# Performance work log

Measured on AMD Instinct MI355X. Metric: run time of the kernel, lower is better.

Reference implementation:

```python
import jax, jax.numpy as jnp
import numpy as np
import math

D = 1024      # input/embed dim
H = 16        # heads
HD = D // H   # head dim
FF = 4096     # feedforward dim
B, S = 2, 2048
LN_EPS = 1e-5
NEG = -9e15


def setup_inputs() -> dict:
    key = jax.random.key(0)
    ks = jax.random.split(key, 16)
    inp = {
        "x": jax.random.normal(ks[0], (B, S, D), jnp.float32),
        "mask": jax.random.randint(ks[1], (1, 1, S, S), 0, 2, jnp.int32),
        "pos_bias": jax.random.normal(ks[2], (1, H, S, S), jnp.float32),
        "sinusoidal_pos": jax.random.normal(ks[3], (1, 1, S, HD), jnp.float32),
        # params (xavier-ish scale)
        "Wqkv": jax.random.normal(ks[4], (D, 3 * D), jnp.float32) * math.sqrt(2.0 / (D + 3 * D)),
        "bqkv": jnp.zeros((3 * D,), jnp.float32),
        "Wo": jax.random.normal(ks[5], (D, D), jnp.float32) * math.sqrt(1.0 / D),
        "bo": jnp.zeros((D,), jnp.float32),
        "W1": jax.random.normal(ks[6], (D, FF), jnp.float32) * math.sqrt(2.0 / (D + FF)),
        "b1": jnp.zeros((FF,), jnp.float32),
        "W2": jax.random.normal(ks[7], (FF, D), jnp.float32) * math.sqrt(2.0 / (D + FF)),
        "b2": jnp.zeros((D,), jnp.float32),
        "g1": jnp.ones((D,), jnp.float32),
        "be1": jnp.zeros((D,), jnp.float32),
        "g2": jnp.ones((D,), jnp.float32),
        "be2": jnp.zeros((D,), jnp.float32),
    }
    return inp


def _layernorm(x, g, b):
    mu = jnp.mean(x, axis=-1, keepdims=True)
    var = jnp.mean(jnp.square(x - mu), axis=-1, keepdims=True)
    return (x - mu) * jax.lax.rsqrt(var + LN_EPS) * g + b


def _rotate_half(x):
    # x: [..., HD] -> reshape [..., 2, HD//2], swap with negation, concat
    r = x.reshape(*x.shape[:-1], 2, -1)
    x1, x2 = r[..., 0, :], r[..., 1, :]
    return jnp.concatenate([-x2, x1], axis=-1)


def _rope(x, sp):
    # sp: [1,1,S,HD]; x: [B,H,S,HD]
    return x * jnp.cos(sp) + _rotate_half(x) * jnp.sin(sp)


def reference(x, mask, pos_bias, sinusoidal_pos, Wqkv, bqkv, Wo, bo,
              W1, b1, W2, b2, g1, be1, g2, be2):
    # pre-norm (note: residual uses the normalized x, matching the source)
    x = _layernorm(x, g1, be1)
    b, s, d = x.shape
    qkv = (x @ Wqkv + bqkv).reshape(b, s, H, 3 * HD).transpose(0, 2, 1, 3)
    q, k, v = jnp.split(qkv, 3, axis=-1)  # each [B,H,S,HD]
    sp = sinusoidal_pos[:, :, -s:]
    q = _rope(q, sp)
    k = _rope(k, sp)
    logits = jnp.einsum("bhqd,bhkd->bhqk", q, k)
    logits = (logits + pos_bias) / math.sqrt(HD)
    logits = jnp.where(mask == 0, NEG, logits)
    attn = jax.nn.softmax(logits, axis=-1)
    vals = jnp.einsum("bhqk,bhkd->bhqd", attn, v)
    vals = vals.transpose(0, 2, 1, 3).reshape(b, s, d)
    attn_out = vals @ Wo + bo
    x = x + attn_out
    x = _layernorm(x, g2, be2)
    h = jax.nn.gelu(x @ W1 + b1, approximate=False)  # torch GELU is exact
    x = x + (h @ W2 + b2)
    return x
```

## Files before the change

kernel.cpp:

```cpp
#include <hip/hip_runtime.h>
#include <math.h>

#define DD   1024
#define HH   16
#define HDD  64
#define FFF  4096
#define NB   2
#define NS   2048
#define NR   (NB * NS)
#define TDQ  (3 * DD)
#define NKT  (NS / 64)

typedef __attribute__((ext_vector_type(8))) _Float16 hfrag;
typedef __attribute__((ext_vector_type(4))) _Float16 h4v;
typedef __attribute__((ext_vector_type(16))) float f32x16;
typedef __attribute__((ext_vector_type(8))) unsigned short us8;
typedef __attribute__((ext_vector_type(4))) unsigned int u32x4;

__device__ __forceinline__ float4 ld4(const float* p) {
    return *reinterpret_cast<const float4*>(p);
}
__device__ __forceinline__ float gelu_f(float x) {
    return 0.5f * x * (1.0f + erff(x * 0.70710678118654752440f));
}
#define MFMA32H(a, b, c) __builtin_amdgcn_mfma_f32_32x32x16_f16((a), (b), (c), 0, 0, 0)

__global__ __launch_bounds__(256) void ln_kernel(const float* __restrict__ in,
        const float* __restrict__ gw, const float* __restrict__ bw,
        float* __restrict__ outf, _Float16* __restrict__ oh) {
    int row = blockIdx.x;
    float4 v = reinterpret_cast<const float4*>(in + (size_t)row * DD)[threadIdx.x];
    float s1 = v.x + v.y + v.z + v.w;
    float s2 = v.x * v.x + v.y * v.y + v.z * v.z + v.w * v.w;
#pragma unroll
    for (int off = 1; off < 64; off <<= 1) {
        s1 += __shfl_xor(s1, off);
        s2 += __shfl_xor(s2, off);
    }
    __shared__ float r1[4], r2[4];
    int wid = threadIdx.x >> 6;
    if ((threadIdx.x & 63) == 0) { r1[wid] = s1; r2[wid] = s2; }
    __syncthreads();
    s1 = r1[0] + r1[1] + r1[2] + r1[3];
    s2 = r2[0] + r2[1] + r2[2] + r2[3];
    float mu   = s1 * (1.0f / DD);
    float var  = s2 * (1.0f / DD) - mu * mu;
    float rstd = rsqrtf(var + 1e-5f);
    float4 g = reinterpret_cast<const float4*>(gw)[threadIdx.x];
    float4 b = reinterpret_cast<const float4*>(bw)[threadIdx.x];
    float o[4];
    o[0] = (v.x - mu) * rstd * g.x + b.x;
    o[1] = (v.y - mu) * rstd * g.y + b.y;
    o[2] = (v.z - mu) * rstd * g.z + b.z;
    o[3] = (v.w - mu) * rstd * g.w + b.w;
    float4 of; of.x = o[0]; of.y = o[1]; of.z = o[2]; of.w = o[3];
    reinterpret_cast<float4*>(outf + (size_t)row * DD)[threadIdx.x] = of;
    h4v hv;
#pragma unroll
    for (int j = 0; j < 4; ++j) hv[j] = (_Float16)o[j];
    *reinterpret_cast<h4v*>(oh + (size_t)row * DD + threadIdx.x * 4) = hv;
}

__global__ __launch_bounds__(256) void wt_convert(const float* __restrict__ W,
        _Float16* __restrict__ Th, int K, int N) {
    __shared__ float s[32][33];
    int tx = threadIdx.x & 31, ty = threadIdx.x >> 5;
    int n0 = blockIdx.x * 32, k0 = blockIdx.y * 32;
#pragma unroll
    for (int i = 0; i < 4; ++i)
        s[ty + i * 8][tx] = W[(size_t)(k0 + ty + i * 8) * N + n0 + tx];
    __syncthreads();
#pragma unroll
    for (int i = 0; i < 4; ++i) {
        int n = n0 + ty + i * 8;
        Th[(size_t)n * K + k0 + tx] = (_Float16)s[tx][ty + i * 8];
    }
}

__global__ __launch_bounds__(256) void cs_table(const float* __restrict__ sp,
        float* __restrict__ ct, float* __restrict__ st) {
    int i = blockIdx.x * 256 + threadIdx.x;
    float v = sp[i];
    ct[i] = cosf(v);
    st[i] = sinf(v);
}

__global__ __launch_bounds__(256) void mask8(const int* __restrict__ mask,
        unsigned char* __restrict__ mb) {
    int i = blockIdx.x * 256 + threadIdx.x;
    int4 v = reinterpret_cast<const int4*>(mask)[i];
    unsigned int o = (unsigned int)(v.x & 1) | ((unsigned int)(v.y & 1) << 8)
                   | ((unsigned int)(v.z & 1) << 16) | ((unsigned int)(v.w & 1) << 24);
    reinterpret_cast<unsigned int*>(mb)[i] = o;
}

__global__ __launch_bounds__(256) void rope_split(const _Float16* __restrict__ qkv,
        const float* __restrict__ ct, const float* __restrict__ st,
        _Float16* __restrict__ Qp, _Float16* __restrict__ Kp, _Float16* __restrict__ Vt) {
    __shared__ _Float16 sv[64][72];
    const int t = threadIdx.x;
    const int tile = blockIdx.x, bh = blockIdx.y;
    const int b = bh >> 4, h = bh & 15;
    const int r = t >> 2, p = t & 3;
    const int srow = tile * 64 + r;
    const _Float16* base = qkv + ((size_t)(b * NS + srow)) * TDQ + h * 192;

#pragma unroll
    for (int qk = 0; qk < 2; ++qk) {
        const _Float16* src = base + qk * 64;
        hfrag va = *reinterpret_cast<const hfrag*>(src + p * 8);
        hfrag vc = *reinterpret_cast<const hfrag*>(src + 32 + p * 8);
        hfrag o1, o2;
#pragma unroll
        for (int j = 0; j < 8; ++j) {
            int d1 = p * 8 + j, d2 = 32 + p * 8 + j;
            float a = (float)va[j], c = (float)vc[j];
            float c1 = ct[(size_t)srow * HDD + d1], s1 = st[(size_t)srow * HDD + d1];
            float c2 = ct[(size_t)srow * HDD + d2], s2 = st[(size_t)srow * HDD + d2];
            o1[j] = (_Float16)(a * c1 - c * s1);
            o2[j] = (_Float16)(c * c2 + a * s2);
        }
        _Float16* dst = qk ? Kp : Qp;
        size_t obase = ((size_t)bh * NS + srow) * HDD;
        *reinterpret_cast<hfrag*>(dst + obase + p * 8)      = o1;
        *reinterpret_cast<hfrag*>(dst + obase + 32 + p * 8) = o2;
    }
    const _Float16* vsrc = base + 128;
    hfrag v0 = *reinterpret_cast<const hfrag*>(vsrc + p * 16);
    hfrag v1 = *reinterpret_cast<const hfrag*>(vsrc + p * 16 + 8);
#pragma unroll
    for (int j = 0; j < 8; ++j) {
        sv[p * 16 + j][r]     = v0[j];
        sv[p * 16 + 8 + j][r] = v1[j];
    }
    __syncthreads();
    {
        int d = t >> 2, kb = (t & 3) * 16;
        size_t obase = ((size_t)bh * HDD + d) * NS + tile * 64 + kb;
        *reinterpret_cast<hfrag*>(Vt + obase)     = *reinterpret_cast<hfrag*>(&sv[d][kb]);
        *reinterpret_cast<hfrag*>(Vt + obase + 8) = *reinterpret_cast<hfrag*>(&sv[d][kb + 8]);
    }
}

__global__ __launch_bounds__(256) void attn_mfma(
        const _Float16* __restrict__ Qp, const _Float16* __restrict__ Kp,
        const _Float16* __restrict__ Vt,
        const float* __restrict__ pos_bias, const unsigned char* __restrict__ maskb,
        float* __restrict__ Opart, float2* __restrict__ Lpart) {
    __shared__ _Float16 kT[64][72];
    __shared__ _Float16 vT[64][72];
    __shared__ _Float16 PBs[4][32][68];
    const int t = threadIdx.x;
    const int w = t >> 6, lane = t & 63, lq = lane & 31, hi = lane >> 5;
    const int h = blockIdx.y >> 1, b = blockIdx.y & 1;
    const int bh = b * HH + h;
    const int qt = blockIdx.x, sp = blockIdx.z;
    const int q0 = qt * 128;
    const int qg = q0 + 32 * w + lq;
    const int sw = ((lq >> 3) & 3) << 3;
    const int KT0 = sp * 16, KT1 = KT0 + 16;
    const float C1  = 0.18033688011112042f;
    const float THR = 11.5f;

    hfrag qf[4];
#pragma unroll
    for (int dk = 0; dk < 4; ++dk)
        qf[dk] = *reinterpret_cast<const hfrag*>(
            Qp + ((size_t)bh * NS + qg) * HDD + 16 * dk + 8 * hi);

    f32x16 o0 = (f32x16)0.0f, o1 = (f32x16)0.0f;
    float mrun = -INFINITY, lsum = 0.0f;

    const int sr0 = t >> 2, sc = t & 3;
    const int swr = ((sr0 >> 3) & 3) << 3;
    const int brow = lane >> 4;
    const int bcol = (lane & 15) * 4;
    us8 kr[2], vr[2];
    float4 pbr[8]; unsigned int pmk[8];

#define STAGE_LOAD(KT) {                                                        \
        int kv0_ = (KT) * 64;                                                   \
        size_t kb_ = ((size_t)bh * NS + kv0_ + sr0) * HDD + 16 * sc;            \
        size_t vb_ = ((size_t)bh * HDD + sr0) * NS + kv0_ + 16 * sc;            \
        kr[0] = *reinterpret_cast<const us8*>(Kp + kb_);                        \
        kr[1] = *reinterpret_cast<const us8*>(Kp + kb_ + 8);                    \
        vr[0] = *reinterpret_cast<const us8*>(Vt + vb_);                        \
        vr[1] = *reinterpret_cast<const us8*>(Vt + vb_ + 8);                    \
        _Pragma("unroll")                                                       \
        for (int i = 0; i < 8; ++i) {                                           \
            int rg_ = q0 + 32 * w + brow + 4 * i;                               \
            pbr[i] = ld4(pos_bias + ((size_t)h * NS + rg_) * NS + kv0_ + bcol); \
            pmk[i] = *reinterpret_cast<const unsigned int*>(                    \
                         maskb + (size_t)rg_ * NS + kv0_ + bcol);               \
        }                                                                       \
    }

    STAGE_LOAD(KT0);
    for (int kt = KT0; kt < KT1; ++kt) {
        __syncthreads();
        *reinterpret_cast<us8*>(&kT[sr0][(16 * sc) ^ swr])     = kr[0];
        *reinterpret_cast<us8*>(&kT[sr0][(16 * sc + 8) ^ swr]) = kr[1];
        *reinterpret_cast<us8*>(&vT[sr0][(16 * sc) ^ swr])     = vr[0];
        *reinterpret_cast<us8*>(&vT[sr0][(16 * sc + 8) ^ swr]) = vr[1];
#pragma unroll
        for (int i = 0; i < 8; ++i) {
            h4v pv;
#pragma unroll
            for (int j = 0; j < 4; ++j)
                pv[j] = ((pmk[i] >> (8 * j)) & 0xffu)
                      ? (_Float16)(pbr[i][j] * C1) : (_Float16)(-60000.0f);
            *reinterpret_cast<h4v*>(&PBs[w][brow + 4 * i][bcol]) = pv;
        }
        __syncthreads();
        if (kt + 1 < KT1) STAGE_LOAD(kt + 1);

        f32x16 s0 = (f32x16)0.0f, s1 = (f32x16)0.0f;
#pragma unroll
        for (int dk = 0; dk < 4; ++dk) {
            hfrag k0 = *reinterpret_cast<const hfrag*>(&kT[lq][(16 * dk + 8 * hi) ^ sw]);
            hfrag k1 = *reinterpret_cast<const hfrag*>(&kT[32 + lq][(16 * dk + 8 * hi) ^ sw]);
            s0 = MFMA32H(k0, qf[dk], s0);
            s1 = MFMA32H(k1, qf[dk], s1);
        }
        float sv[2][16];
#pragma unroll
        for (int m2 = 0; m2 < 2; ++m2)
#pragma unroll
            for (int g = 0; g < 4; ++g) {
                h4v pb4 = *reinterpret_cast<const h4v*>(&PBs[w][lq][32 * m2 + 8 * g + 4 * hi]);
#pragma unroll
                for (int j = 0; j < 4; ++j) {
                    int r = 4 * g + j;
                    float sraw = (m2 == 0) ? s0[r] : s1[r];
                    sv[m2][r] = fmaf(sraw, C1, (float)pb4[j]);
                }
            }
        float mx = sv[0][0];
#pragma unroll
        for (int m2 = 0; m2 < 2; ++m2)
#pragma unroll
            for (int r = 0; r < 16; ++r) mx = fmaxf(mx, sv[m2][r]);
        mx = fmaxf(mx, __shfl_xor(mx, 32));
        if (__any(mx > mrun + THR)) {
            float mnew = fmaxf(mrun, mx);
            float corr = __builtin_amdgcn_exp2f(mrun - mnew);
            lsum *= corr;
            mrun = mnew;
#pragma unroll
            for (int r = 0; r < 16; ++r) {
                int iq = (r & 3) + 8 * (r >> 2) + 4 * hi;
                float cr = __shfl(corr, iq);
                o0[r] *= cr; o1[r] *= cr;
            }
        }
        float ps = 0.0f;
        hfrag af[4];
#pragma unroll
        for (int m2 = 0; m2 < 2; ++m2)
#pragma unroll
            for (int gp = 0; gp < 2; ++gp) {
                float p0 = __builtin_amdgcn_exp2f(sv[m2][8 * gp + 0] - mrun);
                float p1 = __builtin_amdgcn_exp2f(sv[m2][8 * gp + 1] - mrun);
                float p2 = __builtin_amdgcn_exp2f(sv[m2][8 * gp + 2] - mrun);
                float p3 = __builtin_amdgcn_exp2f(sv[m2][8 * gp + 3] - mrun);
                float p4 = __builtin_amdgcn_exp2f(sv[m2][8 * gp + 4] - mrun);
                float p5 = __builtin_amdgcn_exp2f(sv[m2][8 * gp + 5] - mrun);
                float p6 = __builtin_amdgcn_exp2f(sv[m2][8 * gp + 6] - mrun);
                float p7 = __builtin_amdgcn_exp2f(sv[m2][8 * gp + 7] - mrun);
                ps += (p0 + p1) + (p2 + p3) + (p4 + p5) + (p6 + p7);
                unsigned int XA = __builtin_bit_cast(unsigned int, __builtin_amdgcn_cvt_pkrtz(p0, p1));
                unsigned int XB = __builtin_bit_cast(unsigned int, __builtin_amdgcn_cvt_pkrtz(p2, p3));
                unsigned int XC = __builtin_bit_cast(unsigned int, __builtin_amdgcn_cvt_pkrtz(p4, p5));
                unsigned int XD = __builtin_bit_cast(unsigned int, __builtin_amdgcn_cvt_pkrtz(p6, p7));
                unsigned int YA = (unsigned int)__shfl_xor((int)XA, 32);
                unsigned int YB = (unsigned int)__shfl_xor((int)XB, 32);
                unsigned int YC = (unsigned int)__shfl_xor((int)XC, 32);
                unsigned int YD = (unsigned int)__shfl_xor((int)XD, 32);
                u32x4 aw;
                aw[0] = hi ? YC : XA;
                aw[1] = hi ? YD : XB;
                aw[2] = hi ? XC : YA;
                aw[3] = hi ? XD : YB;
                af[m2 * 2 + gp] = __builtin_bit_cast(hfrag, aw);
            }
        ps += __shfl_xor(ps, 32);
        lsum += ps;
#pragma unroll
        for (int kp = 0; kp < 4; ++kp) {
            hfrag v0 = *reinterpret_cast<const hfrag*>(&vT[lq][(16 * kp + 8 * hi) ^ sw]);
            hfrag v1 = *reinterpret_cast<const hfrag*>(&vT[32 + lq][(16 * kp + 8 * hi) ^ sw]);
            o0 = MFMA32H(af[kp], v0, o0);
            o1 = MFMA32H(af[kp], v1, o1);
        }
    }
#undef STAGE_LOAD
    size_t obase = (((size_t)(bh * 16 + qt)) * 2 + sp) * (size_t)(128 * 64);
#pragma unroll
    for (int r = 0; r < 16; ++r) {
        int iq = (r & 3) + 8 * (r >> 2) + 4 * hi;
        Opart[obase + (size_t)(32 * w + iq) * 64 + lq]      = o0[r];
        Opart[obase + (size_t)(32 * w + iq) * 64 + 32 + lq] = o1[r];
    }
    if (hi == 0) {
        float2 ml; ml.x = mrun; ml.y = lsum;
        Lpart[(((size_t)(bh * 16 + qt)) * 2 + sp) * 128 + 32 * w + lq] = ml;
    }
}

__global__ __launch_bounds__(256) void attn_combine(const float* __restrict__ Opart,
        const float2* __restrict__ Lpart, _Float16* __restrict__ valf) {
    const int qt = blockIdx.x;
    const int h = blockIdx.y >> 1, b = blockIdx.y & 1;
    const int bh = b * HH + h;
    const int t = threadIdx.x;
    const int qloc = t >> 2, d0 = (t & 3) * 16;
    size_t base = ((size_t)(bh * 16 + qt)) * 2;
#pragma unroll
    for (int half = 0; half < 2; ++half) {
        int q = qloc + 64 * half;
        float2 ml0 = Lpart[(base + 0) * 128 + q];
        float2 ml1 = Lpart[(base + 1) * 128 + q];
        float m = fmaxf(ml0.x, ml1.x);
        float a0 = __builtin_amdgcn_exp2f(ml0.x - m);
        float a1 = __builtin_amdgcn_exp2f(ml1.x - m);
        float inv = 1.0f / (ml0.y * a0 + ml1.y * a1);
        const float* O0 = Opart + (base + 0) * 8192 + (size_t)q * 64 + d0;
        const float* O1 = Opart + (base + 1) * 8192 + (size_t)q * 64 + d0;
        _Float16* dst = valf + ((size_t)(b * NS + qt * 128 + q)) * DD + h * HDD + d0;
#pragma unroll
        for (int j = 0; j < 4; ++j) {
            float4 x0 = ld4(O0 + 4 * j), x1 = ld4(O1 + 4 * j);
            h4v o;
            o[0] = (_Float16)((x0.x * a0 + x1.x * a1) * inv);
            o[1] = (_Float16)((x0.y * a0 + x1.y * a1) * inv);
            o[2] = (_Float16)((x0.z * a0 + x1.z * a1) * inv);
            o[3] = (_Float16)((x0.w * a0 + x1.w * a1) * inv);
            *reinterpret_cast<h4v*>(dst + 4 * j) = o;
        }
    }
}

template<int EPI>
__global__ __launch_bounds__(256, 2) void gemm_h(
        const _Float16* __restrict__ A, const _Float16* __restrict__ B,
        const float* __restrict__ bias, const float* __restrict__ resid,
        float* __restrict__ Cf, _Float16* __restrict__ Ch,
        int M, int N, int K) {
    __shared__ _Float16 sA[128][72];
    __shared__ _Float16 sB[128][72];
    const int t = threadIdx.x;
    const int w = t >> 6, lane = t & 63, lq = lane & 31, hi = lane >> 5;
    const int wr = w >> 1, wc = w & 1;
    const int m0 = blockIdx.y * 128, n0 = blockIdx.x * 128;
    const int sw = ((lq >> 3) & 3) << 3;

    f32x16 acc[2][2];
#pragma unroll
    for (int m = 0; m < 2; ++m)
#pragma unroll
        for (int n = 0; n < 2; ++n) acc[m][n] = (f32x16)0.0f;

    const int sr = t >> 1, skc = (t & 1) * 16;
    const int swr = ((sr >> 3) & 3) << 3;
    const _Float16* Ap = A + (size_t)(m0 + sr) * K + skc;
    const _Float16* Bp = B + (size_t)(n0 + sr) * K + skc;

    for (int k0 = 0; k0 < K; k0 += 32) {
        us8 a0 = *reinterpret_cast<const us8*>(Ap + k0);
        us8 a1 = *reinterpret_cast<const us8*>(Ap + k0 + 8);
        us8 b0 = *reinterpret_cast<const us8*>(Bp + k0);
        us8 b1 = *reinterpret_cast<const us8*>(Bp + k0 + 8);
        __syncthreads();
        *reinterpret_cast<us8*>(&sA[sr][(skc) ^ swr])     = a0;
        *reinterpret_cast<us8*>(&sA[sr][(skc + 8) ^ swr]) = a1;
        *reinterpret_cast<us8*>(&sB[sr][(skc) ^ swr])     = b0;
        *reinterpret_cast<us8*>(&sB[sr][(skc + 8) ^ swr]) = b1;
        __syncthreads();
        hfrag fa[2][2], fb[2][2];
#pragma unroll
        for (int mb = 0; mb < 2; ++mb)
#pragma unroll
            for (int kc = 0; kc < 2; ++kc)
                fa[mb][kc] = *reinterpret_cast<const hfrag*>(
                    &sA[wr * 64 + mb * 32 + lq][(kc * 16 + 8 * hi) ^ sw]);
#pragma unroll
        for (int nb = 0; nb < 2; ++nb)
#pragma unroll
            for (int kc = 0; kc < 2; ++kc)
                fb[nb][kc] = *reinterpret_cast<const hfrag*>(
                    &sB[wc * 64 + nb * 32 + lq][(kc * 16 + 8 * hi) ^ sw]);
#pragma unroll
        for (int kc = 0; kc < 2; ++kc)
#pragma unroll
            for (int mb = 0; mb < 2; ++mb)
#pragma unroll
                for (int nb = 0; nb < 2; ++nb)
                    acc[mb][nb] = MFMA32H(fa[mb][kc], fb[nb][kc], acc[mb][nb]);
    }
#pragma unroll
    for (int mb = 0; mb < 2; ++mb)
#pragma unroll
        for (int nb = 0; nb < 2; ++nb) {
            int colg = n0 + wc * 64 + nb * 32 + lq;
            float bv = bias[colg];
#pragma unroll
            for (int r = 0; r < 16; ++r) {
                int rowg = m0 + wr * 64 + mb * 32 + (r & 3) + 8 * (r >> 2) + 4 * hi;
                float v = acc[mb][nb][r] + bv;
                if (EPI == 1) v += resid[(size_t)rowg * N + colg];
                if (EPI == 2) {
                    Ch[(size_t)rowg * N + colg] = (_Float16)gelu_f(v);
                } else if (EPI == 3) {
                    Ch[(size_t)rowg * N + colg] = (_Float16)v;
                } else {
                    Cf[(size_t)rowg * N + colg] = v;
                }
            }
        }
}

__global__ __launch_bounds__(256, 2) void gemm_h2(
        const _Float16* __restrict__ A, const _Float16* __restrict__ B,
        const float* __restrict__ bias, const float* __restrict__ resid,
        float* __restrict__ Cf, int M, int N, int K) {
    __shared__ _Float16 sA[64][72];
    __shared__ _Float16 sB[128][72];
    const int t = threadIdx.x;
    const int w = t >> 6, lane = t & 63, lq = lane & 31, hi = lane >> 5;
    const int m0 = blockIdx.y * 64, n0 = blockIdx.x * 128;
    const int sw = ((lq >> 3) & 3) << 3;

    f32x16 acc[2];
    acc[0] = (f32x16)0.0f; acc[1] = (f32x16)0.0f;

    const int ar = t >> 2, akc = (t & 3) * 8;
    const int aswr = ((ar >> 3) & 3) << 3;
    const int br = t >> 1, bkc = (t & 1) * 16;
    const int bswr = ((br >> 3) & 3) << 3;
    const _Float16* Ap = A + (size_t)(m0 + ar) * K + akc;
    const _Float16* Bp = B + (size_t)(n0 + br) * K + bkc;

    for (int k0 = 0; k0 < K; k0 += 32) {
        us8 a0 = *reinterpret_cast<const us8*>(Ap + k0);
        us8 b0 = *reinterpret_cast<const us8*>(Bp + k0);
        us8 b1 = *reinterpret_cast<const us8*>(Bp + k0 + 8);
        __syncthreads();
        *reinterpret_cast<us8*>(&sA[ar][(akc) ^ aswr])     = a0;
        *reinterpret_cast<us8*>(&sB[br][(bkc) ^ bswr])     = b0;
        *reinterpret_cast<us8*>(&sB[br][(bkc + 8) ^ bswr]) = b1;
        __syncthreads();
        hfrag fa[2][2], fb[2];
#pragma unroll
        for (int mb = 0; mb < 2; ++mb)
#pragma unroll
            for (int kc = 0; kc < 2; ++kc)
                fa[mb][kc] = *reinterpret_cast<const hfrag*>(
                    &sA[mb * 32 + lq][(kc * 16 + 8 * hi) ^ sw]);
#pragma unroll
        for (int kc = 0; kc < 2; ++kc)
            fb[kc] = *reinterpret_cast<const hfrag*>(
                &sB[32 * w + lq][(kc * 16 + 8 * hi) ^ sw]);
#pragma unroll
        for (int kc = 0; kc < 2; ++kc)
#pragma unroll
            for (int mb = 0; mb < 2; ++mb)
                acc[mb] = MFMA32H(fa[mb][kc], fb[kc], acc[mb]);
    }
    int colg = n0 + 32 * w + lq;
    float bv = bias[colg];
#pragma unroll
    for (int mb = 0; mb < 2; ++mb)
#pragma unroll
        for (int r = 0; r < 16; ++r) {
            int rowg = m0 + mb * 32 + (r & 3) + 8 * (r >> 2) + 4 * hi;
            float v = acc[mb][r] + bv + resid[(size_t)rowg * N + colg];
            Cf[(size_t)rowg * N + colg] = v;
        }
}

extern "C" void kernel_launch(void* const* d_in, const int* in_sizes, int n_in,
                              void* d_out, int out_size, void* d_ws, size_t ws_size,
                              hipStream_t stream) {
    const float* x        = (const float*)d_in[0];
    const int*   mask     = (const int*)d_in[1];
    const float* pos_bias = (const float*)d_in[2];
    const float* sp       = (const float*)d_in[3];
    const float* Wqkv     = (const float*)d_in[4];
    const float* bqkv     = (const float*)d_in[5];
    const float* Wo       = (const float*)d_in[6];
    const float* bo       = (const float*)d_in[7];
    const float* W1       = (const float*)d_in[8];
    const float* b1       = (const float*)d_in[9];
    const float* W2       = (const float*)d_in[10];
    const float* b2       = (const float*)d_in[11];
    const float* g1       = (const float*)d_in[12];
    const float* be1      = (const float*)d_in[13];
    const float* g2       = (const float*)d_in[14];
    const float* be2      = (const float*)d_in[15];
    float* out = (float*)d_out;
    char* wsb = (char*)d_ws;

    float*          xbuf  = (float*)(wsb);
    _Float16*       actF  = (_Float16*)(wsb + ((size_t)16 << 20));
    _Float16*       wT    = (_Float16*)(wsb + ((size_t)24 << 20));
    float*          ct    = (float*)(wsb + ((size_t)32 << 20));
    float*          stb   = (float*)(wsb + ((size_t)33 << 20));
    unsigned char*  mkb   = (unsigned char*)(wsb + ((size_t)34 << 20));
    _Float16*       qkvh  = (_Float16*)(wsb + ((size_t)48 << 20));
    _Float16*       Qp    = (_Float16*)(wsb + ((size_t)72 << 20));
    _Float16*       Kp    = (_Float16*)(wsb + ((size_t)80 << 20));
    _Float16*       Vt    = (_Float16*)(wsb + ((size_t)88 << 20));
    _Float16*       hF    = (_Float16*)(wsb + ((size_t)48 << 20));
    float*          Opart = (float*)(wsb + ((size_t)96 << 20));
    float2*         Lpart = (float2*)(wsb + ((size_t)130 << 20));

    ln_kernel<<<NR, 256, 0, stream>>>(x, g1, be1, xbuf, actF);
    wt_convert<<<dim3(TDQ / 32, DD / 32), 256, 0, stream>>>(Wqkv, wT, DD, TDQ);
    gemm_h<3><<<dim3(TDQ / 128, NR / 128), 256, 0, stream>>>(
        actF, wT, bqkv, nullptr, nullptr, qkvh, NR, TDQ, DD);
    cs_table<<<(NS * HDD) / 256, 256, 0, stream>>>(sp, ct, stb);
    mask8<<<(NS * NS / 4) / 256, 256, 0, stream>>>(mask, mkb);
    rope_split<<<dim3(NS / 64, NB * HH), 256, 0, stream>>>(qkvh, ct, stb, Qp, Kp, Vt);
    attn_mfma<<<dim3(NS / 128, NB * HH, 2), 256, 0, stream>>>(
        Qp, Kp, Vt, pos_bias, mkb, Opart, Lpart);
    attn_combine<<<dim3(NS / 128, NB * HH), 256, 0, stream>>>(Opart, Lpart, actF);
    wt_convert<<<dim3(DD / 32, DD / 32), 256, 0, stream>>>(Wo, wT, DD, DD);
    gemm_h2<<<dim3(DD / 128, NR / 64), 256, 0, stream>>>(
        actF, wT, bo, xbuf, xbuf, NR, DD, DD);
    ln_kernel<<<NR, 256, 0, stream>>>(xbuf, g2, be2, xbuf, actF);
    wt_convert<<<dim3(FFF / 32, DD / 32), 256, 0, stream>>>(W1, wT, DD, FFF);
    gemm_h<2><<<dim3(FFF / 128, NR / 128), 256, 0, stream>>>(
        actF, wT, b1, nullptr, nullptr, hF, NR, FFF, DD);
    wt_convert<<<dim3(DD / 32, FFF / 32), 256, 0, stream>>>(W2, wT, FFF, DD);
    gemm_h2<<<dim3(DD / 128, NR / 64), 256, 0, stream>>>(
        hF, wT, b2, xbuf, out, NR, DD, FFF);
}
```

Measured before the change: 426.2 us.

## Load attention K/V/bias fragments directly to registers; prefetch GEMM tiles

The attention kernel no longer stages K, V and the masked positional bias through shared memory. Each wave loads its MFMA fragments for K and V and its own bias/mask values straight from global memory into registers and prefetches the next tile, which removes both block barriers per KV tile. The mask is now applied in fp32 inside the softmax prologue. The two GEMM kernels gain software prefetch of the next K-slice into registers before the MFMA loop. This trades LDS reuse across the four waves for redundant global K/V reads and higher register pressure.

```diff
diff --git a/kernel.cpp b/kernel.cpp
--- a/kernel.cpp
+++ b/kernel.cpp
@@ -10,6 +10,7 @@
 #define NR   (NB * NS)
 #define TDQ  (3 * DD)
 #define NKT  (NS / 64)
+#define NSP  2
 
 typedef __attribute__((ext_vector_type(8))) _Float16 hfrag;
 typedef __attribute__((ext_vector_type(4))) _Float16 h4v;
@@ -147,9 +148,6 @@
         const _Float16* __restrict__ Vt,
         const float* __restrict__ pos_bias, const unsigned char* __restrict__ maskb,
         float* __restrict__ Opart, float2* __restrict__ Lpart) {
-    __shared__ _Float16 kT[64][72];
-    __shared__ _Float16 vT[64][72];
-    __shared__ _Float16 PBs[4][32][68];
     const int t = threadIdx.x;
     const int w = t >> 6, lane = t & 63, lq = lane & 31, hi = lane >> 5;
     const int h = blockIdx.y >> 1, b = blockIdx.y & 1;
@@ -157,10 +155,15 @@
     const int qt = blockIdx.x, sp = blockIdx.z;
     const int q0 = qt * 128;
     const int qg = q0 + 32 * w + lq;
-    const int sw = ((lq >> 3) & 3) << 3;
-    const int KT0 = sp * 16, KT1 = KT0 + 16;
-    const float C1  = 0.18033688011112042f;
-    const float THR = 11.5f;
+    const int KT0 = sp * (NKT / NSP), KT1 = KT0 + (NKT / NSP);
+    const float C1   = 0.18033688011112042f;
+    const float NEGL = -1.0e15f;
+    const float THR  = 11.5f;
+
+    const _Float16* kB = Kp + (size_t)bh * NS * HDD;
+    const _Float16* vB = Vt + (size_t)bh * HDD * NS;
+    const float* bB = pos_bias + ((size_t)h * NS + qg) * NS;
+    const unsigned char* mB = maskb + (size_t)qg * NS;
 
     hfrag qf[4];
 #pragma unroll
@@ -171,70 +174,64 @@
     f32x16 o0 = (f32x16)0.0f, o1 = (f32x16)0.0f;
     float mrun = -INFINITY, lsum = 0.0f;
 
-    const int sr0 = t >> 2, sc = t & 3;
-    const int swr = ((sr0 >> 3) & 3) << 3;
-    const int brow = lane >> 4;
-    const int bcol = (lane & 15) * 4;
-    us8 kr[2], vr[2];
+    hfrag kf0[4], kf1[4], vf0[4], vf1[4];
     float4 pbr[8]; unsigned int pmk[8];
 
-#define STAGE_LOAD(KT) {                                                        \
-        int kv0_ = (KT) * 64;                                                   \
-        size_t kb_ = ((size_t)bh * NS + kv0_ + sr0) * HDD + 16 * sc;            \
-        size_t vb_ = ((size_t)bh * HDD + sr0) * NS + kv0_ + 16 * sc;            \
-        kr[0] = *reinterpret_cast<const us8*>(Kp + kb_);                        \
-        kr[1] = *reinterpret_cast<const us8*>(Kp + kb_ + 8);                    \
-        vr[0] = *reinterpret_cast<const us8*>(Vt + vb_);                        \
-        vr[1] = *reinterpret_cast<const us8*>(Vt + vb_ + 8);                    \
-        _Pragma("unroll")                                                       \
-        for (int i = 0; i < 8; ++i) {                                           \
-            int rg_ = q0 + 32 * w + brow + 4 * i;                               \
-            pbr[i] = ld4(pos_bias + ((size_t)h * NS + rg_) * NS + kv0_ + bcol); \
-            pmk[i] = *reinterpret_cast<const unsigned int*>(                    \
-                         maskb + (size_t)rg_ * NS + kv0_ + bcol);               \
-        }                                                                       \
-    }
-
-    STAGE_LOAD(KT0);
+#define LOAD_K(KT) { int kv0_ = (KT) * 64;                                       \
+        _Pragma("unroll")                                                        \
+        for (int dk = 0; dk < 4; ++dk) {                                         \
+            kf0[dk] = *reinterpret_cast<const hfrag*>(                           \
+                kB + (size_t)(kv0_ + lq) * HDD + 16 * dk + 8 * hi);              \
+            kf1[dk] = *reinterpret_cast<const hfrag*>(                           \
+                kB + (size_t)(kv0_ + 32 + lq) * HDD + 16 * dk + 8 * hi);         \
+        } }
+#define LOAD_V(KT) { int kv0_ = (KT) * 64;                                       \
+        _Pragma("unroll")                                                        \
+        for (int kp = 0; kp < 4; ++kp) {                                         \
+            vf0[kp] = *reinterpret_cast<const hfrag*>(                           \
+                vB + (size_t)lq * NS + kv0_ + 16 * kp + 8 * hi);                 \
+            vf1[kp] = *reinterpret_cast<const hfrag*>(                           \
+                vB + (size_t)(32 + lq) * NS + kv0_ + 16 * kp + 8 * hi);          \
+        } }
+#define LOAD_B(KT) { int kv0_ = (KT) * 64;                                       \
+        _Pragma("unroll")                                                        \
+        for (int i = 0; i < 8; ++i) {                                            \
+            int kc_ = kv0_ + 32 * (i >> 2) + 8 * (i & 3) + 4 * hi;               \
+            pbr[i] = ld4(bB + kc_);                                              \
+            pmk[i] = *reinterpret_cast<const unsigned int*>(mB + kc_);           \
+        } }
+
+    LOAD_K(KT0);
+    LOAD_B(KT0);
+    LOAD_V(KT0);
     for (int kt = KT0; kt < KT1; ++kt) {
-        __syncthreads();
-        *reinterpret_cast<us8*>(&kT[sr0][(16 * sc) ^ swr])     = kr[0];
-        *reinterpret_cast<us8*>(&kT[sr0][(16 * sc + 8) ^ swr]) = kr[1];
-        *reinterpret_cast<us8*>(&vT[sr0][(16 * sc) ^ swr])     = vr[0];
-        *reinterpret_cast<us8*>(&vT[sr0][(16 * sc + 8) ^ swr]) = vr[1];
-#pragma unroll
-        for (int i = 0; i < 8; ++i) {
-            h4v pv;
-#pragma unroll
-            for (int j = 0; j < 4; ++j)
-                pv[j] = ((pmk[i] >> (8 * j)) & 0xffu)
-                      ? (_Float16)(pbr[i][j] * C1) : (_Float16)(-60000.0f);
-            *reinterpret_cast<h4v*>(&PBs[w][brow + 4 * i][bcol]) = pv;
-        }
-        __syncthreads();
-        if (kt + 1 < KT1) STAGE_LOAD(kt + 1);
+        const int ktn = (kt + 1 < KT1) ? kt + 1 : kt;
 
         f32x16 s0 = (f32x16)0.0f, s1 = (f32x16)0.0f;
 #pragma unroll
         for (int dk = 0; dk < 4; ++dk) {
-            hfrag k0 = *reinterpret_cast<const hfrag*>(&kT[lq][(16 * dk + 8 * hi) ^ sw]);
-            hfrag k1 = *reinterpret_cast<const hfrag*>(&kT[32 + lq][(16 * dk + 8 * hi) ^ sw]);
-            s0 = MFMA32H(k0, qf[dk], s0);
-            s1 = MFMA32H(k1, qf[dk], s1);
-        }
+            s0 = MFMA32H(kf0[dk], qf[dk], s0);
+            s1 = MFMA32H(kf1[dk], qf[dk], s1);
+        }
+        LOAD_K(ktn);
+
         float sv[2][16];
 #pragma unroll
         for (int m2 = 0; m2 < 2; ++m2)
 #pragma unroll
             for (int g = 0; g < 4; ++g) {
-                h4v pb4 = *reinterpret_cast<const h4v*>(&PBs[w][lq][32 * m2 + 8 * g + 4 * hi]);
+                float4 pb4 = pbr[m2 * 4 + g];
+                unsigned int mk = pmk[m2 * 4 + g];
 #pragma unroll
                 for (int j = 0; j < 4; ++j) {
                     int r = 4 * g + j;
                     float sraw = (m2 == 0) ? s0[r] : s1[r];
-                    sv[m2][r] = fmaf(sraw, C1, (float)pb4[j]);
+                    sv[m2][r] = ((mk >> (8 * j)) & 0xffu)
+                              ? (sraw + pb4[j]) * C1 : NEGL;
                 }
             }
+        LOAD_B(ktn);
+
         float mx = sv[0][0];
 #pragma unroll
         for (int m2 = 0; m2 < 2; ++m2)
@@ -287,14 +284,15 @@
         lsum += ps;
 #pragma unroll
         for (int kp = 0; kp < 4; ++kp) {
-            hfrag v0 = *reinterpret_cast<const hfrag*>(&vT[lq][(16 * kp + 8 * hi) ^ sw]);
-            hfrag v1 = *reinterpret_cast<const hfrag*>(&vT[32 + lq][(16 * kp + 8 * hi) ^ sw]);
-            o0 = MFMA32H(af[kp], v0, o0);
-            o1 = MFMA32H(af[kp], v1, o1);
-        }
-    }
-#undef STAGE_LOAD
-    size_t obase = (((size_t)(bh * 16 + qt)) * 2 + sp) * (size_t)(128 * 64);
+            o0 = MFMA32H(af[kp], vf0[kp], o0);
+            o1 = MFMA32H(af[kp], vf1[kp], o1);
+        }
+        LOAD_V(ktn);
+    }
+#undef LOAD_K
+#undef LOAD_V
+#undef LOAD_B
+    size_t obase = (((size_t)(bh * 16 + qt)) * NSP + sp) * (size_t)(128 * 64);
 #pragma unroll
     for (int r = 0; r < 16; ++r) {
         int iq = (r & 3) + 8 * (r >> 2) + 4 * hi;
@@ -303,7 +301,7 @@
     }
     if (hi == 0) {
         float2 ml; ml.x = mrun; ml.y = lsum;
-        Lpart[(((size_t)(bh * 16 + qt)) * 2 + sp) * 128 + 32 * w + lq] = ml;
+        Lpart[(((size_t)(bh * 16 + qt)) * NSP + sp) * 128 + 32 * w + lq] = ml;
     }
 }
 
@@ -314,7 +312,7 @@
     const int bh = b * HH + h;
     const int t = threadIdx.x;
     const int qloc = t >> 2, d0 = (t & 3) * 16;
-    size_t base = ((size_t)(bh * 16 + qt)) * 2;
+    size_t base = ((size_t)(bh * 16 + qt)) * NSP;
 #pragma unroll
     for (int half = 0; half < 2; ++half) {
         int q = qloc + 64 * half;
@@ -365,17 +363,22 @@
     const _Float16* Ap = A + (size_t)(m0 + sr) * K + skc;
     const _Float16* Bp = B + (size_t)(n0 + sr) * K + skc;
 
+    us8 a0, a1, b0, b1;
+#define GEMM_LOAD(KOFF) {                                         \
+        a0 = *reinterpret_cast<const us8*>(Ap + (KOFF));          \
+        a1 = *reinterpret_cast<const us8*>(Ap + (KOFF) + 8);      \
+        b0 = *reinterpret_cast<const us8*>(Bp + (KOFF));          \
+        b1 = *reinterpret_cast<const us8*>(Bp + (KOFF) + 8);      \
+    }
+    GEMM_LOAD(0);
     for (int k0 = 0; k0 < K; k0 += 32) {
-        us8 a0 = *reinterpret_cast<const us8*>(Ap + k0);
-        us8 a1 = *reinterpret_cast<const us8*>(Ap + k0 + 8);
-        us8 b0 = *reinterpret_cast<const us8*>(Bp + k0);
-        us8 b1 = *reinterpret_cast<const us8*>(Bp + k0 + 8);
         __syncthreads();
         *reinterpret_cast<us8*>(&sA[sr][(skc) ^ swr])     = a0;
         *reinterpret_cast<us8*>(&sA[sr][(skc + 8) ^ swr]) = a1;
         *reinterpret_cast<us8*>(&sB[sr][(skc) ^ swr])     = b0;
         *reinterpret_cast<us8*>(&sB[sr][(skc + 8) ^ swr]) = b1;
         __syncthreads();
+        if (k0 + 32 < K) GEMM_LOAD(k0 + 32);
         hfrag fa[2][2], fb[2][2];
 #pragma unroll
         for (int mb = 0; mb < 2; ++mb)
@@ -397,6 +400,7 @@
                 for (int nb = 0; nb < 2; ++nb)
                     acc[mb][nb] = MFMA32H(fa[mb][kc], fb[nb][kc], acc[mb][nb]);
     }
+#undef GEMM_LOAD
 #pragma unroll
     for (int mb = 0; mb < 2; ++mb)
 #pragma unroll
@@ -440,15 +444,20 @@
     const _Float16* Ap = A + (size_t)(m0 + ar) * K + akc;
     const _Float16* Bp = B + (size_t)(n0 + br) * K + bkc;
 
+    us8 a0, b0, b1;
+#define GEMM2_LOAD(KOFF) {                                        \
+        a0 = *reinterpret_cast<const us8*>(Ap + (KOFF));          \
+        b0 = *reinterpret_cast<const us8*>(Bp + (KOFF));          \
+        b1 = *reinterpret_cast<const us8*>(Bp + (KOFF) + 8);      \
+    }
+    GEMM2_LOAD(0);
     for (int k0 = 0; k0 < K; k0 += 32) {
-        us8 a0 = *reinterpret_cast<const us8*>(Ap + k0);
-        us8 b0 = *reinterpret_cast<const us8*>(Bp + k0);
-        us8 b1 = *reinterpret_cast<const us8*>(Bp + k0 + 8);
         __syncthreads();
         *reinterpret_cast<us8*>(&sA[ar][(akc) ^ aswr])     = a0;
         *reinterpret_cast<us8*>(&sB[br][(bkc) ^ bswr])     = b0;
         *reinterpret_cast<us8*>(&sB[br][(bkc + 8) ^ bswr]) = b1;
         __syncthreads();
+        if (k0 + 32 < K) GEMM2_LOAD(k0 + 32);
         hfrag fa[2][2], fb[2];
 #pragma unroll
         for (int mb = 0; mb < 2; ++mb)
@@ -466,6 +475,7 @@
             for (int mb = 0; mb < 2; ++mb)
                 acc[mb] = MFMA32H(fa[mb][kc], fb[kc], acc[mb]);
     }
+#undef GEMM2_LOAD
     int colg = n0 + 32 * w + lq;
     float bv = bias[colg];
 #pragma unroll
@@ -521,7 +531,7 @@
     cs_table<<<(NS * HDD) / 256, 256, 0, stream>>>(sp, ct, stb);
     mask8<<<(NS * NS / 4) / 256, 256, 0, stream>>>(mask, mkb);
     rope_split<<<dim3(NS / 64, NB * HH), 256, 0, stream>>>(qkvh, ct, stb, Qp, Kp, Vt);
-    attn_mfma<<<dim3(NS / 128, NB * HH, 2), 256, 0, stream>>>(
+    attn_mfma<<<dim3(NS / 128, NB * HH, NSP), 256, 0, stream>>>(
         Qp, Kp, Vt, pos_bias, mkb, Opart, Lpart);
     attn_combine<<<dim3(NS / 128, NB * HH), 256, 0, stream>>>(Opart, Lpart, actF);
     wt_convert<<<dim3(DD / 32, DD / 32), 256, 0, stream>>>(Wo, wT, DD, DD);
```

After: 509.2 us. 1.19x slower.

## Double-buffer GEMM tiles with direct global-to-LDS loads

Applied to the files above, without the earlier changes.

Both GEMM kernels now stage A/B tiles with global_load_lds straight into LDS and double-buffer them, prefetching the next k-slice while MFMAs run on the current one. This leaves one barrier per iteration instead of two and drops the register round trip. The padded XOR-swizzled layout becomes an unpadded 32-wide layout, which risks LDS bank conflicts on fragment reads, and the two-blocks-per-CU launch bound is removed. The attention split count becomes a named constant with the same value, so attention is unchanged.

```diff
diff --git a/kernel.cpp b/kernel.cpp
--- a/kernel.cpp
+++ b/kernel.cpp
@@ -10,6 +10,7 @@
 #define NR   (NB * NS)
 #define TDQ  (3 * DD)
 #define NKT  (NS / 64)
+#define NSP  2
 
 typedef __attribute__((ext_vector_type(8))) _Float16 hfrag;
 typedef __attribute__((ext_vector_type(4))) _Float16 h4v;
@@ -22,6 +23,11 @@
 }
 __device__ __forceinline__ float gelu_f(float x) {
     return 0.5f * x * (1.0f + erff(x * 0.70710678118654752440f));
+}
+__device__ __forceinline__ void gld16(const void* g, void* l) {
+    __builtin_amdgcn_global_load_lds(
+        (const __attribute__((address_space(1))) unsigned int*)g,
+        (__attribute__((address_space(3))) unsigned int*)l, 16, 0, 0);
 }
 #define MFMA32H(a, b, c) __builtin_amdgcn_mfma_f32_32x32x16_f16((a), (b), (c), 0, 0, 0)
 
@@ -158,7 +164,7 @@
     const int q0 = qt * 128;
     const int qg = q0 + 32 * w + lq;
     const int sw = ((lq >> 3) & 3) << 3;
-    const int KT0 = sp * 16, KT1 = KT0 + 16;
+    const int KT0 = sp * (NKT / NSP), KT1 = KT0 + (NKT / NSP);
     const float C1  = 0.18033688011112042f;
     const float THR = 11.5f;
 
@@ -294,7 +300,7 @@
         }
     }
 #undef STAGE_LOAD
-    size_t obase = (((size_t)(bh * 16 + qt)) * 2 + sp) * (size_t)(128 * 64);
+    size_t obase = (((size_t)(bh * 16 + qt)) * NSP + sp) * (size_t)(128 * 64);
 #pragma unroll
     for (int r = 0; r < 16; ++r) {
         int iq = (r & 3) + 8 * (r >> 2) + 4 * hi;
@@ -303,7 +309,7 @@
     }
     if (hi == 0) {
         float2 ml; ml.x = mrun; ml.y = lsum;
-        Lpart[(((size_t)(bh * 16 + qt)) * 2 + sp) * 128 + 32 * w + lq] = ml;
+        Lpart[(((size_t)(bh * 16 + qt)) * NSP + sp) * 128 + 32 * w + lq] = ml;
     }
 }
 
@@ -314,7 +320,7 @@
     const int bh = b * HH + h;
     const int t = threadIdx.x;
     const int qloc = t >> 2, d0 = (t & 3) * 16;
-    size_t base = ((size_t)(bh * 16 + qt)) * 2;
+    size_t base = ((size_t)(bh * 16 + qt)) * NSP;
 #pragma unroll
     for (int half = 0; half < 2; ++half) {
         int q = qloc + 64 * half;
@@ -341,18 +347,17 @@
 }
 
 template<int EPI>
-__global__ __launch_bounds__(256, 2) void gemm_h(
+__global__ __launch_bounds__(256) void gemm_h(
         const _Float16* __restrict__ A, const _Float16* __restrict__ B,
         const float* __restrict__ bias, const float* __restrict__ resid,
         float* __restrict__ Cf, _Float16* __restrict__ Ch,
         int M, int N, int K) {
-    __shared__ _Float16 sA[128][72];
-    __shared__ _Float16 sB[128][72];
+    __shared__ _Float16 sA[2][128][32];
+    __shared__ _Float16 sB[2][128][32];
     const int t = threadIdx.x;
     const int w = t >> 6, lane = t & 63, lq = lane & 31, hi = lane >> 5;
     const int wr = w >> 1, wc = w & 1;
     const int m0 = blockIdx.y * 128, n0 = blockIdx.x * 128;
-    const int sw = ((lq >> 3) & 3) << 3;
 
     f32x16 acc[2][2];
 #pragma unroll
@@ -360,35 +365,37 @@
 #pragma unroll
         for (int n = 0; n < 2; ++n) acc[m][n] = (f32x16)0.0f;
 
-    const int sr = t >> 1, skc = (t & 1) * 16;
-    const int swr = ((sr >> 3) & 3) << 3;
-    const _Float16* Ap = A + (size_t)(m0 + sr) * K + skc;
-    const _Float16* Bp = B + (size_t)(n0 + sr) * K + skc;
-
+    const int r0 = t >> 2, c0 = (t & 3) * 8;
+    const _Float16* ApG0 = A + (size_t)(m0 + r0) * K + c0;
+    const _Float16* ApG1 = A + (size_t)(m0 + 64 + r0) * K + c0;
+    const _Float16* BpG0 = B + (size_t)(n0 + r0) * K + c0;
+    const _Float16* BpG1 = B + (size_t)(n0 + 64 + r0) * K + c0;
+
+#define STAGE(KOFF, BUF) {                                   \
+        gld16(ApG0 + (KOFF), &sA[BUF][r0][c0]);              \
+        gld16(ApG1 + (KOFF), &sA[BUF][64 + r0][c0]);         \
+        gld16(BpG0 + (KOFF), &sB[BUF][r0][c0]);              \
+        gld16(BpG1 + (KOFF), &sB[BUF][64 + r0][c0]);         \
+    }
+
+    STAGE(0, 0);
+    __syncthreads();
+    int cur = 0;
     for (int k0 = 0; k0 < K; k0 += 32) {
-        us8 a0 = *reinterpret_cast<const us8*>(Ap + k0);
-        us8 a1 = *reinterpret_cast<const us8*>(Ap + k0 + 8);
-        us8 b0 = *reinterpret_cast<const us8*>(Bp + k0);
-        us8 b1 = *reinterpret_cast<const us8*>(Bp + k0 + 8);
-        __syncthreads();
-        *reinterpret_cast<us8*>(&sA[sr][(skc) ^ swr])     = a0;
-        *reinterpret_cast<us8*>(&sA[sr][(skc + 8) ^ swr]) = a1;
-        *reinterpret_cast<us8*>(&sB[sr][(skc) ^ swr])     = b0;
-        *reinterpret_cast<us8*>(&sB[sr][(skc + 8) ^ swr]) = b1;
-        __syncthreads();
+        if (k0 + 32 < K) STAGE(k0 + 32, cur ^ 1);
         hfrag fa[2][2], fb[2][2];
 #pragma unroll
         for (int mb = 0; mb < 2; ++mb)
 #pragma unroll
             for (int kc = 0; kc < 2; ++kc)
                 fa[mb][kc] = *reinterpret_cast<const hfrag*>(
-                    &sA[wr * 64 + mb * 32 + lq][(kc * 16 + 8 * hi) ^ sw]);
+                    &sA[cur][wr * 64 + mb * 32 + lq][kc * 16 + 8 * hi]);
 #pragma unroll
         for (int nb = 0; nb < 2; ++nb)
 #pragma unroll
             for (int kc = 0; kc < 2; ++kc)
                 fb[nb][kc] = *reinterpret_cast<const hfrag*>(
-                    &sB[wc * 64 + nb * 32 + lq][(kc * 16 + 8 * hi) ^ sw]);
+                    &sB[cur][wc * 64 + nb * 32 + lq][kc * 16 + 8 * hi]);
 #pragma unroll
         for (int kc = 0; kc < 2; ++kc)
 #pragma unroll
@@ -396,7 +403,10 @@
 #pragma unroll
                 for (int nb = 0; nb < 2; ++nb)
                     acc[mb][nb] = MFMA32H(fa[mb][kc], fb[nb][kc], acc[mb][nb]);
-    }
+        __syncthreads();
+        cur ^= 1;
+    }
+#undef STAGE
 #pragma unroll
     for (int mb = 0; mb < 2; ++mb)
 #pragma unroll
@@ -419,53 +429,55 @@
         }
 }
 
-__global__ __launch_bounds__(256, 2) void gemm_h2(
+__global__ __launch_bounds__(256) void gemm_h2(
         const _Float16* __restrict__ A, const _Float16* __restrict__ B,
         const float* __restrict__ bias, const float* __restrict__ resid,
         float* __restrict__ Cf, int M, int N, int K) {
-    __shared__ _Float16 sA[64][72];
-    __shared__ _Float16 sB[128][72];
+    __shared__ _Float16 sA[2][64][32];
+    __shared__ _Float16 sB[2][128][32];
     const int t = threadIdx.x;
     const int w = t >> 6, lane = t & 63, lq = lane & 31, hi = lane >> 5;
     const int m0 = blockIdx.y * 64, n0 = blockIdx.x * 128;
-    const int sw = ((lq >> 3) & 3) << 3;
 
     f32x16 acc[2];
     acc[0] = (f32x16)0.0f; acc[1] = (f32x16)0.0f;
 
-    const int ar = t >> 2, akc = (t & 3) * 8;
-    const int aswr = ((ar >> 3) & 3) << 3;
-    const int br = t >> 1, bkc = (t & 1) * 16;
-    const int bswr = ((br >> 3) & 3) << 3;
-    const _Float16* Ap = A + (size_t)(m0 + ar) * K + akc;
-    const _Float16* Bp = B + (size_t)(n0 + br) * K + bkc;
-
+    const int r0 = t >> 2, c0 = (t & 3) * 8;
+    const _Float16* ApG0 = A + (size_t)(m0 + r0) * K + c0;
+    const _Float16* BpG0 = B + (size_t)(n0 + r0) * K + c0;
+    const _Float16* BpG1 = B + (size_t)(n0 + 64 + r0) * K + c0;
+
+#define STAGE2(KOFF, BUF) {                                  \
+        gld16(ApG0 + (KOFF), &sA[BUF][r0][c0]);              \
+        gld16(BpG0 + (KOFF), &sB[BUF][r0][c0]);              \
+        gld16(BpG1 + (KOFF), &sB[BUF][64 + r0][c0]);         \
+    }
+
+    STAGE2(0, 0);
+    __syncthreads();
+    int cur = 0;
     for (int k0 = 0; k0 < K; k0 += 32) {
-        us8 a0 = *reinterpret_cast<const us8*>(Ap + k0);
-        us8 b0 = *reinterpret_cast<const us8*>(Bp + k0);
-        us8 b1 = *reinterpret_cast<const us8*>(Bp + k0 + 8);
-        __syncthreads();
-        *reinterpret_cast<us8*>(&sA[ar][(akc) ^ aswr])     = a0;
-        *reinterpret_cast<us8*>(&sB[br][(bkc) ^ bswr])     = b0;
-        *reinterpret_cast<us8*>(&sB[br][(bkc + 8) ^ bswr]) = b1;
-        __syncthreads();
+        if (k0 + 32 < K) STAGE2(k0 + 32, cur ^ 1);
         hfrag fa[2][2], fb[2];
 #pragma unroll
         for (int mb = 0; mb < 2; ++mb)
 #pragma unroll
             for (int kc = 0; kc < 2; ++kc)
                 fa[mb][kc] = *reinterpret_cast<const hfrag*>(
-                    &sA[mb * 32 + lq][(kc * 16 + 8 * hi) ^ sw]);
+                    &sA[cur][mb * 32 + lq][kc * 16 + 8 * hi]);
 #pragma unroll
         for (int kc = 0; kc < 2; ++kc)
             fb[kc] = *reinterpret_cast<const hfrag*>(
-                &sB[32 * w + lq][(kc * 16 + 8 * hi) ^ sw]);
+                &sB[cur][32 * w + lq][kc * 16 + 8 * hi]);
 #pragma unroll
         for (int kc = 0; kc < 2; ++kc)
 #pragma unroll
             for (int mb = 0; mb < 2; ++mb)
                 acc[mb] = MFMA32H(fa[mb][kc], fb[kc], acc[mb]);
-    }
+        __syncthreads();
+        cur ^= 1;
+    }
+#undef STAGE2
     int colg = n0 + 32 * w + lq;
     float bv = bias[colg];
 #pragma unroll
@@ -521,7 +533,7 @@
     cs_table<<<(NS * HDD) / 256, 256, 0, stream>>>(sp, ct, stb);
     mask8<<<(NS * NS / 4) / 256, 256, 0, stream>>>(mask, mkb);
     rope_split<<<dim3(NS / 64, NB * HH), 256, 0, stream>>>(qkvh, ct, stb, Qp, Kp, Vt);
-    attn_mfma<<<dim3(NS / 128, NB * HH, 2), 256, 0, stream>>>(
+    attn_mfma<<<dim3(NS / 128, NB * HH, NSP), 256, 0, stream>>>(
         Qp, Kp, Vt, pos_bias, mkb, Opart, Lpart);
     attn_combine<<<dim3(NS / 128, NB * HH), 256, 0, stream>>>(Opart, Lpart, actF);
     wt_convert<<<dim3(DD / 32, DD / 32), 256, 0, stream>>>(Wo, wT, DD, DD);
```

Result: slower. 435.7 us (+2.2%).

## Widen gemm_h tile to 128x256 and register-prefetch next K slice in GEMMs

Applied to the files above, without the earlier changes.

The main gemm_h kernel's N tile is doubled to 256 columns, so each warp computes a 64x128 output with 8 accumulators, and the grids for the QKV and FF1 GEMMs are halved to match. Both GEMM kernels now load the next K slice from global memory into registers right after the shared-memory barrier, overlapping that load with the MFMA work of the current slice. The attention split count is parameterized as NSP but kept at 2. The wider tile raises register and LDS use and drops the two-blocks-per-CU launch bound, which may lower occupancy and leave fewer blocks for the QKV GEMM.

```diff
diff --git a/kernel.cpp b/kernel.cpp
--- a/kernel.cpp
+++ b/kernel.cpp
@@ -10,6 +10,7 @@
 #define NR   (NB * NS)
 #define TDQ  (3 * DD)
 #define NKT  (NS / 64)
+#define NSP  2
 
 typedef __attribute__((ext_vector_type(8))) _Float16 hfrag;
 typedef __attribute__((ext_vector_type(4))) _Float16 h4v;
@@ -158,7 +159,7 @@
     const int q0 = qt * 128;
     const int qg = q0 + 32 * w + lq;
     const int sw = ((lq >> 3) & 3) << 3;
-    const int KT0 = sp * 16, KT1 = KT0 + 16;
+    const int KT0 = sp * (NKT / NSP), KT1 = KT0 + (NKT / NSP);
     const float C1  = 0.18033688011112042f;
     const float THR = 11.5f;
 
@@ -294,7 +295,7 @@
         }
     }
 #undef STAGE_LOAD
-    size_t obase = (((size_t)(bh * 16 + qt)) * 2 + sp) * (size_t)(128 * 64);
+    size_t obase = (((size_t)(bh * 16 + qt)) * NSP + sp) * (size_t)(128 * 64);
 #pragma unroll
     for (int r = 0; r < 16; ++r) {
         int iq = (r & 3) + 8 * (r >> 2) + 4 * hi;
@@ -303,7 +304,7 @@
     }
     if (hi == 0) {
         float2 ml; ml.x = mrun; ml.y = lsum;
-        Lpart[(((size_t)(bh * 16 + qt)) * 2 + sp) * 128 + 32 * w + lq] = ml;
+        Lpart[(((size_t)(bh * 16 + qt)) * NSP + sp) * 128 + 32 * w + lq] = ml;
     }
 }
 
@@ -314,7 +315,7 @@
     const int bh = b * HH + h;
     const int t = threadIdx.x;
     const int qloc = t >> 2, d0 = (t & 3) * 16;
-    size_t base = ((size_t)(bh * 16 + qt)) * 2;
+    size_t base = ((size_t)(bh * 16 + qt)) * NSP;
 #pragma unroll
     for (int half = 0; half < 2; ++half) {
         int q = qloc + 64 * half;
@@ -341,42 +342,53 @@
 }
 
 template<int EPI>
-__global__ __launch_bounds__(256, 2) void gemm_h(
+__global__ __launch_bounds__(256) void gemm_h(
         const _Float16* __restrict__ A, const _Float16* __restrict__ B,
         const float* __restrict__ bias, const float* __restrict__ resid,
         float* __restrict__ Cf, _Float16* __restrict__ Ch,
         int M, int N, int K) {
     __shared__ _Float16 sA[128][72];
-    __shared__ _Float16 sB[128][72];
+    __shared__ _Float16 sB[256][72];
     const int t = threadIdx.x;
     const int w = t >> 6, lane = t & 63, lq = lane & 31, hi = lane >> 5;
     const int wr = w >> 1, wc = w & 1;
-    const int m0 = blockIdx.y * 128, n0 = blockIdx.x * 128;
+    const int m0 = blockIdx.y * 128, n0 = blockIdx.x * 256;
     const int sw = ((lq >> 3) & 3) << 3;
 
-    f32x16 acc[2][2];
+    f32x16 acc[2][4];
 #pragma unroll
     for (int m = 0; m < 2; ++m)
 #pragma unroll
-        for (int n = 0; n < 2; ++n) acc[m][n] = (f32x16)0.0f;
+        for (int n = 0; n < 4; ++n) acc[m][n] = (f32x16)0.0f;
 
     const int sr = t >> 1, skc = (t & 1) * 16;
-    const int swr = ((sr >> 3) & 3) << 3;
+    const int swrA = ((sr >> 3) & 3) << 3;
+    const int br = t;
+    const int swrB = ((br >> 3) & 3) << 3;
     const _Float16* Ap = A + (size_t)(m0 + sr) * K + skc;
-    const _Float16* Bp = B + (size_t)(n0 + sr) * K + skc;
-
+    const _Float16* Bp = B + (size_t)(n0 + br) * K;
+
+    us8 a0, a1, b0, b1, b2, b3;
+#define GEMM_LOAD(KOFF) {                                         \
+        a0 = *reinterpret_cast<const us8*>(Ap + (KOFF));          \
+        a1 = *reinterpret_cast<const us8*>(Ap + (KOFF) + 8);      \
+        b0 = *reinterpret_cast<const us8*>(Bp + (KOFF));          \
+        b1 = *reinterpret_cast<const us8*>(Bp + (KOFF) + 8);      \
+        b2 = *reinterpret_cast<const us8*>(Bp + (KOFF) + 16);     \
+        b3 = *reinterpret_cast<const us8*>(Bp + (KOFF) + 24);     \
+    }
+    GEMM_LOAD(0);
     for (int k0 = 0; k0 < K; k0 += 32) {
-        us8 a0 = *reinterpret_cast<const us8*>(Ap + k0);
-        us8 a1 = *reinterpret_cast<const us8*>(Ap + k0 + 8);
-        us8 b0 = *reinterpret_cast<const us8*>(Bp + k0);
-        us8 b1 = *reinterpret_cast<const us8*>(Bp + k0 + 8);
         __syncthreads();
-        *reinterpret_cast<us8*>(&sA[sr][(skc) ^ swr])     = a0;
-        *reinterpret_cast<us8*>(&sA[sr][(skc + 8) ^ swr]) = a1;
-        *reinterpret_cast<us8*>(&sB[sr][(skc) ^ swr])     = b0;
-        *reinterpret_cast<us8*>(&sB[sr][(skc + 8) ^ swr]) = b1;
+        *reinterpret_cast<us8*>(&sA[sr][(skc) ^ swrA])     = a0;
+        *reinterpret_cast<us8*>(&sA[sr][(skc + 8) ^ swrA]) = a1;
+        *reinterpret_cast<us8*>(&sB[br][(0) ^ swrB])       = b0;
+        *reinterpret_cast<us8*>(&sB[br][(8) ^ swrB])       = b1;
+        *reinterpret_cast<us8*>(&sB[br][(16) ^ swrB])      = b2;
+        *reinterpret_cast<us8*>(&sB[br][(24) ^ swrB])      = b3;
         __syncthreads();
-        hfrag fa[2][2], fb[2][2];
+        if (k0 + 32 < K) GEMM_LOAD(k0 + 32);
+        hfrag fa[2][2], fb[4][2];
 #pragma unroll
         for (int mb = 0; mb < 2; ++mb)
 #pragma unroll
@@ -384,24 +396,25 @@
                 fa[mb][kc] = *reinterpret_cast<const hfrag*>(
                     &sA[wr * 64 + mb * 32 + lq][(kc * 16 + 8 * hi) ^ sw]);
 #pragma unroll
-        for (int nb = 0; nb < 2; ++nb)
+        for (int nb = 0; nb < 4; ++nb)
 #pragma unroll
             for (int kc = 0; kc < 2; ++kc)
                 fb[nb][kc] = *reinterpret_cast<const hfrag*>(
-                    &sB[wc * 64 + nb * 32 + lq][(kc * 16 + 8 * hi) ^ sw]);
+                    &sB[wc * 128 + nb * 32 + lq][(kc * 16 + 8 * hi) ^ sw]);
 #pragma unroll
         for (int kc = 0; kc < 2; ++kc)
 #pragma unroll
             for (int mb = 0; mb < 2; ++mb)
 #pragma unroll
-                for (int nb = 0; nb < 2; ++nb)
+                for (int nb = 0; nb < 4; ++nb)
                     acc[mb][nb] = MFMA32H(fa[mb][kc], fb[nb][kc], acc[mb][nb]);
     }
+#undef GEMM_LOAD
 #pragma unroll
     for (int mb = 0; mb < 2; ++mb)
 #pragma unroll
-        for (int nb = 0; nb < 2; ++nb) {
-            int colg = n0 + wc * 64 + nb * 32 + lq;
+        for (int nb = 0; nb < 4; ++nb) {
+            int colg = n0 + wc * 128 + nb * 32 + lq;
             float bv = bias[colg];
 #pragma unroll
             for (int r = 0; r < 16; ++r) {
@@ -440,15 +453,20 @@
     const _Float16* Ap = A + (size_t)(m0 + ar) * K + akc;
     const _Float16* Bp = B + (size_t)(n0 + br) * K + bkc;
 
+    us8 a0, b0, b1;
+#define GEMM2_LOAD(KOFF) {                                        \
+        a0 = *reinterpret_cast<const us8*>(Ap + (KOFF));          \
+        b0 = *reinterpret_cast<const us8*>(Bp + (KOFF));          \
+        b1 = *reinterpret_cast<const us8*>(Bp + (KOFF) + 8);      \
+    }
+    GEMM2_LOAD(0);
     for (int k0 = 0; k0 < K; k0 += 32) {
-        us8 a0 = *reinterpret_cast<const us8*>(Ap + k0);
-        us8 b0 = *reinterpret_cast<const us8*>(Bp + k0);
-        us8 b1 = *reinterpret_cast<const us8*>(Bp + k0 + 8);
         __syncthreads();
         *reinterpret_cast<us8*>(&sA[ar][(akc) ^ aswr])     = a0;
         *reinterpret_cast<us8*>(&sB[br][(bkc) ^ bswr])     = b0;
         *reinterpret_cast<us8*>(&sB[br][(bkc + 8) ^ bswr]) = b1;
         __syncthreads();
+        if (k0 + 32 < K) GEMM2_LOAD(k0 + 32);
         hfrag fa[2][2], fb[2];
 #pragma unroll
         for (int mb = 0; mb < 2; ++mb)
@@ -466,6 +484,7 @@
             for (int mb = 0; mb < 2; ++mb)
                 acc[mb] = MFMA32H(fa[mb][kc], fb[kc], acc[mb]);
     }
+#undef GEMM2_LOAD
     int colg = n0 + 32 * w + lq;
     float bv = bias[colg];
 #pragma unroll
@@ -516,12 +535,12 @@
 
     ln_kernel<<<NR, 256, 0, stream>>>(x, g1, be1, xbuf, actF);
     wt_convert<<<dim3(TDQ / 32, DD / 32), 256, 0, stream>>>(Wqkv, wT, DD, TDQ);
-    gemm_h<3><<<dim3(TDQ / 128, NR / 128), 256, 0, stream>>>(
+    gemm_h<3><<<dim3(TDQ / 256, NR / 128), 256, 0, stream>>>(
         actF, wT, bqkv, nullptr, nullptr, qkvh, NR, TDQ, DD);
     cs_table<<<(NS * HDD) / 256, 256, 0, stream>>>(sp, ct, stb);
     mask8<<<(NS * NS / 4) / 256, 256, 0, stream>>>(mask, mkb);
     rope_split<<<dim3(NS / 64, NB * HH), 256, 0, stream>>>(qkvh, ct, stb, Qp, Kp, Vt);
-    attn_mfma<<<dim3(NS / 128, NB * HH, 2), 256, 0, stream>>>(
+    attn_mfma<<<dim3(NS / 128, NB * HH, NSP), 256, 0, stream>>>(
         Qp, Kp, Vt, pos_bias, mkb, Opart, Lpart);
     attn_combine<<<dim3(NS / 128, NB * HH), 256, 0, stream>>>(Opart, Lpart, actF);
     wt_convert<<<dim3(DD / 32, DD / 32), 256, 0, stream>>>(Wo, wT, DD, DD);
@@ -529,7 +548,7 @@
         actF, wT, bo, xbuf, xbuf, NR, DD, DD);
     ln_kernel<<<NR, 256, 0, stream>>>(xbuf, g2, be2, xbuf, actF);
     wt_convert<<<dim3(FFF / 32, DD / 32), 256, 0, stream>>>(W1, wT, DD, FFF);
-    gemm_h<2><<<dim3(FFF / 128, NR / 128), 256, 0, stream>>>(
+    gemm_h<2><<<dim3(FFF / 256, NR / 128), 256, 0, stream>>>(
         actF, wT, b1, nullptr, nullptr, hF, NR, FFF, DD);
     wt_convert<<<dim3(DD / 32, FFF / 32), 256, 0, stream>>>(W2, wT, FFF, DD);
     gemm_h2<<<dim3(DD / 128, NR / 64), 256, 0, stream>>>(
```

After: 480.4 us. +12.7%, slower.
